# Optimization experiments

Hardware: AMD Instinct MI355X
Metric: run time of the kernel (lower is better)

Reference implementation:

```python
import jax, jax.numpy as jnp
import numpy as np

E = 4          # num_experts
M = 4          # num_modals
C = 512        # in_channels
H1, H2, OUT = 128, 48, 16  # expert hidden/output channels


def setup_inputs() -> dict:
    key = jax.random.key(0)
    ks = jax.random.split(key, 8)
    b, n, t = 16, 4096, 1

    def w(k, shape, fan_in):
        return jax.random.normal(k, shape, jnp.float32) * (1.0 / np.sqrt(fan_in))

    return {
        "x": jax.random.normal(ks[0], (b, C, M, n, t), jnp.float32),
        # stacked expert params: leading axis = expert
        "W1": w(ks[1], (E, H1, C), C),   "b1": jnp.zeros((E, H1), jnp.float32),
        "W2": w(ks[2], (E, H2, H1), H1), "b2": jnp.zeros((E, H2), jnp.float32),
        "W3": w(ks[3], (E, OUT, H2), H2),"b3": jnp.zeros((E, OUT), jnp.float32),
        # gate params
        "Wg1": w(ks[4], (H1, C), C),     "bg1": jnp.zeros((H1,), jnp.float32),
        "Wg2": w(ks[5], (E, H1), H1),    "bg2": jnp.zeros((E,), jnp.float32),
    }


def reference(x, W1, b1, W2, b2, W3, b3, Wg1, bg1, Wg2, bg2):
    b = x.shape[0]
    # gate: AdaptiveAvgPool3d((M,1,1)) == mean over (n,t) since m==M already
    pooled = x.mean(axis=(3, 4))                                   # (b, C, M)
    g = jax.nn.relu(jnp.einsum('oc,bcm->bom', Wg1, pooled) + bg1[None, :, None])
    g = jnp.einsum('oc,bcm->bom', Wg2, g) + bg2[None, :, None]     # (b, E, M)
    # torch: flatten then view(b, num_modals, num_experts) -> row-major reshape
    weights = jax.nn.softmax(g.reshape(b, M, E), axis=2)           # (b, M, E)

    # all experts densely: 1x1x1 convs == channel matmuls, stacked over e
    h = jax.nn.relu(jnp.einsum('eoc,bcmnt->ebomnt', W1, x)
                    + b1[:, None, :, None, None, None])            # (E,b,H1,M,n,t)
    h = jax.nn.relu(jnp.einsum('eoi,ebimnt->ebomnt', W2, h)
                    + b2[:, None, :, None, None, None])            # (E,b,H2,M,n,t)
    h = (jnp.einsum('eoi,ebimnt->ebomnt', W3, h)
         + b3[:, None, :, None, None, None])                       # (E,b,OUT,M,n,t)

    # per-modal weighted combination over experts
    out = jnp.einsum('ebomnt,bme->bomnt', h, weights)              # (b,OUT,M,n,t)
    return out
```

## Files before the change

kernel.cpp:

```cpp
#include <hip/hip_runtime.h>

typedef _Float16 f16;
typedef f16 f16x8 __attribute__((ext_vector_type(8)));
typedef f16 f16x4 __attribute__((ext_vector_type(4)));
typedef f16 f16x2 __attribute__((ext_vector_type(2)));
typedef float f32x4 __attribute__((ext_vector_type(4)));

#define BDIM 16
#define CDIM 512
#define MDIM 4
#define NDIM 4096
#define NB   64
#define NTILES (NDIM/NB)
#define NBMT  (BDIM*MDIM*NTILES)

#define SX(p) ((((p)&7) ^ (((p)>>3)&7)))

__global__ __launch_bounds__(256) void prep_kernel(
    const float* __restrict__ W1, const float* __restrict__ W2, const float* __restrict__ W3,
    f16* __restrict__ W1s, f16* __restrict__ W2s, f16* __restrict__ W3s)
{
  int i = blockIdx.x * 256 + threadIdx.x;
  if (i < 262144) {
    int ki = i & 7; int rest = i >> 3;
    int o = rest & 127; rest >>= 7;
    int kb = rest & 63; int e = rest >> 6;
    W1s[i] = (f16)W1[(e*128 + o)*512 + kb*8 + ki];
  } else if (i < 262144 + 24576) {
    int j = i - 262144;
    int ki = j & 7; int rest = j >> 3;
    int o = rest % 48; rest /= 48;
    int kb = rest & 15; int e = rest >> 4;
    W2s[j] = (f16)W2[(e*48 + o)*128 + kb*8 + ki];
  } else if (i < 262144 + 24576 + 4096) {
    int j = i - 262144 - 24576;
    int ki = j & 7; int rest = j >> 3;
    int o = rest & 15; rest >>= 4;
    int kb = rest & 7; int e = rest >> 3;
    int k = kb*8 + ki;
    W3s[j] = (k < 48) ? (f16)W3[(e*16 + o)*48 + k] : (f16)0.f;
  }
}

__global__ __launch_bounds__(1024, 4) void moe_kernel(
    const float* __restrict__ x,
    const f16* __restrict__ W1s, const f16* __restrict__ W2s, const f16* __restrict__ W3s,
    const float* __restrict__ b1, const float* __restrict__ b2, const float* __restrict__ b3,
    float* __restrict__ partial, f16* __restrict__ h3)
{
  extern __shared__ char smem[];
  char* H1t = smem;
  char* H2t = smem + 65536;

  const int tid  = threadIdx.x;
  const int bid  = blockIdx.x;
  const int tile = bid & 63;
  const int m    = (bid >> 6) & 3;
  const int b    = bid >> 8;

  const int wave = tid >> 6, lane = tid & 63;
  const int g = lane >> 4, r = lane & 15;
  const int eh = wave >> 3;
  const int o0 = (wave & 7) * 16;

  {
    uint4 z = make_uint4(0u,0u,0u,0u);
    ((uint4*)H2t)[tid] = z;
    ((uint4*)H2t)[tid + 1024] = z;
  }

  const int cp0 = tid >> 4;
  const int q   = tid & 15;
  const size_t xrow = ((size_t)(b*2048 + m))*4096 + (size_t)tile*64 + (size_t)(q*4);

  #pragma unroll
  for (int it = 0; it < 2; ++it) {
    const int cp = cp0 + it*64;
    const int c  = 2*cp;
    f32x4 v0 = *(const f32x4*)(x + xrow + (size_t)c*16384);
    f32x4 v1 = *(const f32x4*)(x + xrow + (size_t)(c+1)*16384);
    #pragma unroll
    for (int i = 0; i < 4; ++i) {
      int p = q*4 + i;
      f16x2 hv; hv[0] = (f16)v0[i]; hv[1] = (f16)v1[i];
      *(f16x2*)(smem + p*512 + ((4*cp) ^ (SX(p)<<4))) = hv;
    }
    float s0 = v0[0]+v0[1]+v0[2]+v0[3];
    float s1 = v1[0]+v1[1]+v1[2]+v1[3];
    #pragma unroll
    for (int off = 8; off; off >>= 1) {
      s0 += __shfl_down(s0, off, 16);
      s1 += __shfl_down(s1, off, 16);
    }
    if (q == 0) { float2 sv = {s0, s1}; *(float2*)(partial + (size_t)bid*512 + c) = sv; }
  }
  __syncthreads();

  f32x4 acc[2][4];
  #pragma unroll
  for (int i = 0; i < 2; ++i)
    #pragma unroll
    for (int pt = 0; pt < 4; ++pt) acc[i][pt] = (f32x4){0.f,0.f,0.f,0.f};

  auto compute_half = [&](const char* Xb, int h) {
    #pragma unroll
    for (int ks = 0; ks < 8; ++ks) {
      const int kbh = ks*4 + g;
      const int kbg = h*32 + kbh;
      f16x8 bf[4];
      #pragma unroll
      for (int pt = 0; pt < 4; ++pt) {
        int p = pt*16 + r;
        bf[pt] = *(const f16x8*)(Xb + p*512 + ((kbh*16) ^ (SX(p)<<4)));
      }
      #pragma unroll
      for (int i = 0; i < 2; ++i) {
        const int e = eh*2 + i;
        f16x8 a = *(const f16x8*)(W1s + ((size_t)((e*64 + kbg)*128) + o0 + r)*8);
        acc[i][0] = __builtin_amdgcn_mfma_f32_16x16x32_f16(a, bf[0], acc[i][0], 0, 0, 0);
        acc[i][1] = __builtin_amdgcn_mfma_f32_16x16x32_f16(a, bf[1], acc[i][1], 0, 0, 0);
        acc[i][2] = __builtin_amdgcn_mfma_f32_16x16x32_f16(a, bf[2], acc[i][2], 0, 0, 0);
        acc[i][3] = __builtin_amdgcn_mfma_f32_16x16x32_f16(a, bf[3], acc[i][3], 0, 0, 0);
      }
    }
  };

  f32x4 nva0, nva1, nvb0, nvb1;
  {
    const int ca = 256 + 2*cp0;
    const int cb = 256 + 2*(cp0 + 64);
    nva0 = *(const f32x4*)(x + xrow + (size_t)ca*16384);
    nva1 = *(const f32x4*)(x + xrow + (size_t)(ca+1)*16384);
    nvb0 = *(const f32x4*)(x + xrow + (size_t)cb*16384);
    nvb1 = *(const f32x4*)(x + xrow + (size_t)(cb+1)*16384);
  }
  compute_half(smem, 0);

  {
    char* X1 = smem + 32768;
    #pragma unroll
    for (int i = 0; i < 4; ++i) {
      int p = q*4 + i;
      f16x2 ha; ha[0] = (f16)nva0[i]; ha[1] = (f16)nva1[i];
      *(f16x2*)(X1 + p*512 + ((4*cp0) ^ (SX(p)<<4))) = ha;
      f16x2 hb; hb[0] = (f16)nvb0[i]; hb[1] = (f16)nvb1[i];
      *(f16x2*)(X1 + p*512 + ((4*(cp0+64)) ^ (SX(p)<<4))) = hb;
    }
    float sa0 = nva0[0]+nva0[1]+nva0[2]+nva0[3];
    float sa1 = nva1[0]+nva1[1]+nva1[2]+nva1[3];
    float sb0 = nvb0[0]+nvb0[1]+nvb0[2]+nvb0[3];
    float sb1 = nvb1[0]+nvb1[1]+nvb1[2]+nvb1[3];
    #pragma unroll
    for (int off = 8; off; off >>= 1) {
      sa0 += __shfl_down(sa0, off, 16);
      sa1 += __shfl_down(sa1, off, 16);
      sb0 += __shfl_down(sb0, off, 16);
      sb1 += __shfl_down(sb1, off, 16);
    }
    if (q == 0) {
      float2 sva = {sa0, sa1};
      float2 svb = {sb0, sb1};
      *(float2*)(partial + (size_t)bid*512 + 256 + 2*cp0)       = sva;
      *(float2*)(partial + (size_t)bid*512 + 256 + 2*(cp0+64))  = svb;
    }
  }
  __syncthreads();
  compute_half(smem + 32768, 1);
  __syncthreads();

  #pragma unroll
  for (int i = 0; i < 2; ++i) {
    const int e = eh*2 + i;
    const f32x4 bias = *(const f32x4*)(b1 + e*128 + o0 + g*4);
    const int colb = (o0 + g*4)*2;
    #pragma unroll
    for (int pt = 0; pt < 4; ++pt) {
      int p = pt*16 + r;
      f16x4 hv;
      #pragma unroll
      for (int j = 0; j < 4; ++j) hv[j] = (f16)fmaxf(acc[i][pt][j] + bias[j], 0.f);
      *(f16x4*)(H1t + e*16384 + p*256 + (colb ^ (SX(p)<<4))) = hv;
    }
  }
  __syncthreads();

  #pragma unroll
  for (int s = 0; s < 3; ++s) {
    const int f  = wave*3 + s;
    const int e  = f / 12;
    const int ot = (f % 12) >> 2;
    const int pt = f & 3;
    const int p  = pt*16 + r;
    f32x4 acc2 = {0.f,0.f,0.f,0.f};
    #pragma unroll
    for (int ks = 0; ks < 4; ++ks) {
      const int kb = ks*4 + g;
      f16x8 a  = *(const f16x8*)(W2s + (size_t)((e*16 + kb)*48 + ot*16 + r)*8);
      f16x8 bf = *(const f16x8*)(H1t + e*16384 + p*256 + ((kb*16) ^ (SX(p)<<4)));
      acc2 = __builtin_amdgcn_mfma_f32_16x16x32_f16(a, bf, acc2, 0, 0, 0);
    }
    const f32x4 bias = *(const f32x4*)(b2 + e*48 + ot*16 + g*4);
    const int colb = (ot*16 + g*4)*2;
    f16x4 hv;
    #pragma unroll
    for (int j = 0; j < 4; ++j) hv[j] = (f16)fmaxf(acc2[j] + bias[j], 0.f);
    *(f16x4*)(H2t + e*8192 + p*128 + (colb ^ (SX(p)<<4))) = hv;
  }
  __syncthreads();

  {
    const int e  = wave >> 2;
    const int pt = wave & 3;
    const int p  = pt*16 + r;
    f32x4 acc3 = {0.f,0.f,0.f,0.f};
    #pragma unroll
    for (int ks = 0; ks < 2; ++ks) {
      const int kb = ks*4 + g;
      f16x8 a  = *(const f16x8*)(W3s + (size_t)((e*8 + kb)*16 + r)*8);
      f16x8 bf = *(const f16x8*)(H2t + e*8192 + p*128 + ((kb*16) ^ (SX(p)<<4)));
      acc3 = __builtin_amdgcn_mfma_f32_16x16x32_f16(a, bf, acc3, 0, 0, 0);
    }
    const f32x4 bias = *(const f32x4*)(b3 + e*16 + g*4);
    #pragma unroll
    for (int j = 0; j < 4; ++j) {
      int o = g*4 + j;
      h3[(((size_t)(e*NBMT + bid))*16 + o)*64 + pt*16 + r] = (f16)(acc3[j] + bias[j]);
    }
  }
}

__global__ __launch_bounds__(256) void gate_kernel(
    const float* __restrict__ partial, const float* __restrict__ Wg1,
    const float* __restrict__ bg1, const float* __restrict__ Wg2,
    const float* __restrict__ bg2, float* __restrict__ wgt)
{
  __shared__ float pl[512*4];
  __shared__ float g1[128*4];
  __shared__ float g2[16];
  const int b = blockIdx.x, tid = threadIdx.x;

  const int c0 = tid * 2;
  #pragma unroll
  for (int mm = 0; mm < 4; ++mm) {
    const float* base = partial + ((size_t)((b*4 + mm)*64))*512 + c0;
    float a0 = 0.f, a1 = 0.f;
    for (int tl = 0; tl < 64; ++tl) {
      float2 v = *(const float2*)(base + tl*512);
      a0 += v.x; a1 += v.y;
    }
    pl[(c0+0)*4 + mm] = a0 * (1.0f/4096.0f);
    pl[(c0+1)*4 + mm] = a1 * (1.0f/4096.0f);
  }
  __syncthreads();

  #pragma unroll
  for (int u = 0; u < 2; ++u) {
    int idx = u*256 + tid;
    int o = idx >> 2, mm = idx & 3;
    float acc = bg1[o];
    for (int c = 0; c < 512; ++c) acc += Wg1[o*512 + c] * pl[c*4 + mm];
    g1[o*4 + mm] = fmaxf(acc, 0.f);
  }
  __syncthreads();
  if (tid < 16) {
    int e = tid >> 2, mm = tid & 3;
    float acc = bg2[e];
    for (int o = 0; o < 128; ++o) acc += Wg2[e*128 + o] * g1[o*4 + mm];
    g2[e*4 + mm] = acc;
  }
  __syncthreads();
  if (tid < 4) {
    int mrow = tid;
    float v0 = g2[mrow*4+0], v1 = g2[mrow*4+1], v2 = g2[mrow*4+2], v3 = g2[mrow*4+3];
    float mx = fmaxf(fmaxf(v0,v1), fmaxf(v2,v3));
    float e0 = expf(v0-mx), e1 = expf(v1-mx), e2 = expf(v2-mx), e3 = expf(v3-mx);
    float inv = 1.0f / (e0+e1+e2+e3);
    wgt[b*16 + mrow*4 + 0] = e0*inv;
    wgt[b*16 + mrow*4 + 1] = e1*inv;
    wgt[b*16 + mrow*4 + 2] = e2*inv;
    wgt[b*16 + mrow*4 + 3] = e3*inv;
  }
}

__global__ __launch_bounds__(256) void combine_kernel(
    const f16* __restrict__ h3, const float* __restrict__ wgt,
    float* __restrict__ out)
{
  const int bmt = blockIdx.x;
  const int tile = bmt & 63, m = (bmt >> 6) & 3, b = bmt >> 8;
  const int t = threadIdx.x;
  const int o = t >> 4, pq = t & 15;

  const f32x4 w = *(const f32x4*)(wgt + (b*4 + m)*4);
  f32x4 s = {0.f, 0.f, 0.f, 0.f};
  #pragma unroll
  for (int e = 0; e < 4; ++e) {
    f16x4 h = *(const f16x4*)(h3 + (((size_t)(e*NBMT + bmt))*16 + o)*64 + pq*4);
    #pragma unroll
    for (int j = 0; j < 4; ++j) s[j] += w[e] * (float)h[j];
  }
  *(f32x4*)(out + (((size_t)b*16 + o)*4 + m)*4096 + tile*64 + pq*4) = s;
}

extern "C" void kernel_launch(void* const* d_in, const int* in_sizes, int n_in,
                              void* d_out, int out_size, void* d_ws, size_t ws_size,
                              hipStream_t stream) {
  const float* x   = (const float*)d_in[0];
  const float* W1  = (const float*)d_in[1];
  const float* b1  = (const float*)d_in[2];
  const float* W2  = (const float*)d_in[3];
  const float* b2  = (const float*)d_in[4];
  const float* W3  = (const float*)d_in[5];
  const float* b3  = (const float*)d_in[6];
  const float* Wg1 = (const float*)d_in[7];
  const float* bg1 = (const float*)d_in[8];
  const float* Wg2 = (const float*)d_in[9];
  const float* bg2 = (const float*)d_in[10];
  float* out = (float*)d_out;

  char* ws = (char*)d_ws;
  float* wgt    = (float*)ws;
  f16* W1s      = (f16*)(ws + 4096);
  f16* W2s      = (f16*)(ws + 4096 + 524288);
  f16* W3s      = (f16*)(ws + 4096 + 524288 + 49152);
  float* partial= (float*)(ws + (1u<<20));
  f16* h3       = (f16*)(ws + (16u<<20));

  hipFuncSetAttribute(reinterpret_cast<const void*>(moe_kernel),
                      hipFuncAttributeMaxDynamicSharedMemorySize, 98304);

  prep_kernel<<<(262144 + 24576 + 4096 + 255)/256, 256, 0, stream>>>(W1, W2, W3, W1s, W2s, W3s);
  moe_kernel<<<NBMT, 1024, 98304, stream>>>(x, W1s, W2s, W3s, b1, b2, b3, partial, h3);
  gate_kernel<<<BDIM, 256, 0, stream>>>(partial, Wg1, bg1, Wg2, bg2, wgt);
  combine_kernel<<<NBMT, 256, 0, stream>>>(h3, wgt, out);
}
```

Before: 419.4 us.

## Pre-transpose x to f16, compute gate first, fuse combine into persistent MoE kernel

A new xprep kernel converts x to an f16 tile-major layout and computes the channel sums for pooling. The gate then runs before the MoE kernel, so the MoE kernel can apply the softmax weights directly and write the final output, removing the h3 intermediate and the combine kernel. The MoE kernel is now persistent: 256 blocks each loop over 16 tiles, double-buffering the next f16 tile from global memory through registers into shared memory. The cost is an extra f16 round trip of x through global memory and fewer blocks, each using more shared memory.

New measurement: 813.7 us. 1.94x slower.

```diff
diff --git a/kernel.cpp b/kernel.cpp
--- a/kernel.cpp
+++ b/kernel.cpp
@@ -3,18 +3,16 @@
 typedef _Float16 f16;
 typedef f16 f16x8 __attribute__((ext_vector_type(8)));
 typedef f16 f16x4 __attribute__((ext_vector_type(4)));
-typedef f16 f16x2 __attribute__((ext_vector_type(2)));
 typedef float f32x4 __attribute__((ext_vector_type(4)));
 
 #define BDIM 16
-#define CDIM 512
 #define MDIM 4
 #define NDIM 4096
 #define NB   64
 #define NTILES (NDIM/NB)
 #define NBMT  (BDIM*MDIM*NTILES)
 
-#define SX(p) ((((p)&7) ^ (((p)>>3)&7)))
+#define MFMA16(a,b,c) __builtin_amdgcn_mfma_f32_16x16x32_f16(a, b, c, 0, 0, 0)
 
 __global__ __launch_bounds__(256) void prep_kernel(
     const float* __restrict__ W1, const float* __restrict__ W2, const float* __restrict__ W3,
@@ -42,191 +40,50 @@
   }
 }
 
-__global__ __launch_bounds__(1024, 4) void moe_kernel(
-    const float* __restrict__ x,
-    const f16* __restrict__ W1s, const f16* __restrict__ W2s, const f16* __restrict__ W3s,
-    const float* __restrict__ b1, const float* __restrict__ b2, const float* __restrict__ b3,
-    float* __restrict__ partial, f16* __restrict__ h3)
+__global__ __launch_bounds__(256) void xprep_kernel(
+    const float* __restrict__ x, f16* __restrict__ Xt, float* __restrict__ partial)
 {
-  extern __shared__ char smem[];
-  char* H1t = smem;
-  char* H2t = smem + 65536;
-
-  const int tid  = threadIdx.x;
-  const int bid  = blockIdx.x;
-  const int tile = bid & 63;
-  const int m    = (bid >> 6) & 3;
-  const int b    = bid >> 8;
-
-  const int wave = tid >> 6, lane = tid & 63;
-  const int g = lane >> 4, r = lane & 15;
-  const int eh = wave >> 3;
-  const int o0 = (wave & 7) * 16;
-
-  {
-    uint4 z = make_uint4(0u,0u,0u,0u);
-    ((uint4*)H2t)[tid] = z;
-    ((uint4*)H2t)[tid + 1024] = z;
-  }
-
-  const int cp0 = tid >> 4;
-  const int q   = tid & 15;
-  const size_t xrow = ((size_t)(b*2048 + m))*4096 + (size_t)tile*64 + (size_t)(q*4);
+  const int bid = blockIdx.x;
+  const int cb  = bid & 63;
+  const int bm  = bid >> 6;
+  const int b   = bm >> 2, m = bm & 3;
+  const int t   = threadIdx.x;
+  const int lane = t & 63, wid = t >> 6;
+
+  __shared__ float red[4][8];
+  float s[8] = {0.f,0.f,0.f,0.f,0.f,0.f,0.f,0.f};
 
   #pragma unroll
-  for (int it = 0; it < 2; ++it) {
-    const int cp = cp0 + it*64;
-    const int c  = 2*cp;
-    f32x4 v0 = *(const f32x4*)(x + xrow + (size_t)c*16384);
-    f32x4 v1 = *(const f32x4*)(x + xrow + (size_t)(c+1)*16384);
+  for (int pass = 0; pass < 4; ++pass) {
+    const int n0 = pass*1024 + t*4;
+    f32x4 v[8];
+    #pragma unroll
+    for (int ci = 0; ci < 8; ++ci)
+      v[ci] = *(const f32x4*)(x + (((size_t)(b*512 + cb*8 + ci))*4 + m)*4096 + n0);
+    #pragma unroll
+    for (int ci = 0; ci < 8; ++ci)
+      s[ci] += v[ci][0] + v[ci][1] + v[ci][2] + v[ci][3];
+    const int tile = n0 >> 6, p = n0 & 63;
+    const size_t obase = (((size_t)bm*64 + tile)*64 + cb)*64;
     #pragma unroll
     for (int i = 0; i < 4; ++i) {
-      int p = q*4 + i;
-      f16x2 hv; hv[0] = (f16)v0[i]; hv[1] = (f16)v1[i];
-      *(f16x2*)(smem + p*512 + ((4*cp) ^ (SX(p)<<4))) = hv;
-    }
-    float s0 = v0[0]+v0[1]+v0[2]+v0[3];
-    float s1 = v1[0]+v1[1]+v1[2]+v1[3];
-    #pragma unroll
-    for (int off = 8; off; off >>= 1) {
-      s0 += __shfl_down(s0, off, 16);
-      s1 += __shfl_down(s1, off, 16);
-    }
-    if (q == 0) { float2 sv = {s0, s1}; *(float2*)(partial + (size_t)bid*512 + c) = sv; }
-  }
+      f16x8 o;
+      #pragma unroll
+      for (int ci = 0; ci < 8; ++ci) o[ci] = (f16)v[ci][i];
+      *(f16x8*)(Xt + (obase + p + i)*8) = o;
+    }
+  }
+
+  #pragma unroll
+  for (int off = 32; off; off >>= 1)
+    #pragma unroll
+    for (int ci = 0; ci < 8; ++ci) s[ci] += __shfl_down(s[ci], off);
+  if (lane == 0)
+    #pragma unroll
+    for (int ci = 0; ci < 8; ++ci) red[wid][ci] = s[ci];
   __syncthreads();
-
-  f32x4 acc[2][4];
-  #pragma unroll
-  for (int i = 0; i < 2; ++i)
-    #pragma unroll
-    for (int pt = 0; pt < 4; ++pt) acc[i][pt] = (f32x4){0.f,0.f,0.f,0.f};
-
-  auto compute_half = [&](const char* Xb, int h) {
-    #pragma unroll
-    for (int ks = 0; ks < 8; ++ks) {
-      const int kbh = ks*4 + g;
-      const int kbg = h*32 + kbh;
-      f16x8 bf[4];
-      #pragma unroll
-      for (int pt = 0; pt < 4; ++pt) {
-        int p = pt*16 + r;
-        bf[pt] = *(const f16x8*)(Xb + p*512 + ((kbh*16) ^ (SX(p)<<4)));
-      }
-      #pragma unroll
-      for (int i = 0; i < 2; ++i) {
-        const int e = eh*2 + i;
-        f16x8 a = *(const f16x8*)(W1s + ((size_t)((e*64 + kbg)*128) + o0 + r)*8);
-        acc[i][0] = __builtin_amdgcn_mfma_f32_16x16x32_f16(a, bf[0], acc[i][0], 0, 0, 0);
-        acc[i][1] = __builtin_amdgcn_mfma_f32_16x16x32_f16(a, bf[1], acc[i][1], 0, 0, 0);
-        acc[i][2] = __builtin_amdgcn_mfma_f32_16x16x32_f16(a, bf[2], acc[i][2], 0, 0, 0);
-        acc[i][3] = __builtin_amdgcn_mfma_f32_16x16x32_f16(a, bf[3], acc[i][3], 0, 0, 0);
-      }
-    }
-  };
-
-  f32x4 nva0, nva1, nvb0, nvb1;
-  {
-    const int ca = 256 + 2*cp0;
-    const int cb = 256 + 2*(cp0 + 64);
-    nva0 = *(const f32x4*)(x + xrow + (size_t)ca*16384);
-    nva1 = *(const f32x4*)(x + xrow + (size_t)(ca+1)*16384);
-    nvb0 = *(const f32x4*)(x + xrow + (size_t)cb*16384);
-    nvb1 = *(const f32x4*)(x + xrow + (size_t)(cb+1)*16384);
-  }
-  compute_half(smem, 0);
-
-  {
-    char* X1 = smem + 32768;
-    #pragma unroll
-    for (int i = 0; i < 4; ++i) {
-      int p = q*4 + i;
-      f16x2 ha; ha[0] = (f16)nva0[i]; ha[1] = (f16)nva1[i];
-      *(f16x2*)(X1 + p*512 + ((4*cp0) ^ (SX(p)<<4))) = ha;
-      f16x2 hb; hb[0] = (f16)nvb0[i]; hb[1] = (f16)nvb1[i];
-      *(f16x2*)(X1 + p*512 + ((4*(cp0+64)) ^ (SX(p)<<4))) = hb;
-    }
-    float sa0 = nva0[0]+nva0[1]+nva0[2]+nva0[3];
-    float sa1 = nva1[0]+nva1[1]+nva1[2]+nva1[3];
-    float sb0 = nvb0[0]+nvb0[1]+nvb0[2]+nvb0[3];
-    float sb1 = nvb1[0]+nvb1[1]+nvb1[2]+nvb1[3];
-    #pragma unroll
-    for (int off = 8; off; off >>= 1) {
-      sa0 += __shfl_down(sa0, off, 16);
-      sa1 += __shfl_down(sa1, off, 16);
-      sb0 += __shfl_down(sb0, off, 16);
-      sb1 += __shfl_down(sb1, off, 16);
-    }
-    if (q == 0) {
-      float2 sva = {sa0, sa1};
-      float2 svb = {sb0, sb1};
-      *(float2*)(partial + (size_t)bid*512 + 256 + 2*cp0)       = sva;
-      *(float2*)(partial + (size_t)bid*512 + 256 + 2*(cp0+64))  = svb;
-    }
-  }
-  __syncthreads();
-  compute_half(smem + 32768, 1);
-  __syncthreads();
-
-  #pragma unroll
-  for (int i = 0; i < 2; ++i) {
-    const int e = eh*2 + i;
-    const f32x4 bias = *(const f32x4*)(b1 + e*128 + o0 + g*4);
-    const int colb = (o0 + g*4)*2;
-    #pragma unroll
-    for (int pt = 0; pt < 4; ++pt) {
-      int p = pt*16 + r;
-      f16x4 hv;
-      #pragma unroll
-      for (int j = 0; j < 4; ++j) hv[j] = (f16)fmaxf(acc[i][pt][j] + bias[j], 0.f);
-      *(f16x4*)(H1t + e*16384 + p*256 + (colb ^ (SX(p)<<4))) = hv;
-    }
-  }
-  __syncthreads();
-
-  #pragma unroll
-  for (int s = 0; s < 3; ++s) {
-    const int f  = wave*3 + s;
-    const int e  = f / 12;
-    const int ot = (f % 12) >> 2;
-    const int pt = f & 3;
-    const int p  = pt*16 + r;
-    f32x4 acc2 = {0.f,0.f,0.f,0.f};
-    #pragma unroll
-    for (int ks = 0; ks < 4; ++ks) {
-      const int kb = ks*4 + g;
-      f16x8 a  = *(const f16x8*)(W2s + (size_t)((e*16 + kb)*48 + ot*16 + r)*8);
-      f16x8 bf = *(const f16x8*)(H1t + e*16384 + p*256 + ((kb*16) ^ (SX(p)<<4)));
-      acc2 = __builtin_amdgcn_mfma_f32_16x16x32_f16(a, bf, acc2, 0, 0, 0);
-    }
-    const f32x4 bias = *(const f32x4*)(b2 + e*48 + ot*16 + g*4);
-    const int colb = (ot*16 + g*4)*2;
-    f16x4 hv;
-    #pragma unroll
-    for (int j = 0; j < 4; ++j) hv[j] = (f16)fmaxf(acc2[j] + bias[j], 0.f);
-    *(f16x4*)(H2t + e*8192 + p*128 + (colb ^ (SX(p)<<4))) = hv;
-  }
-  __syncthreads();
-
-  {
-    const int e  = wave >> 2;
-    const int pt = wave & 3;
-    const int p  = pt*16 + r;
-    f32x4 acc3 = {0.f,0.f,0.f,0.f};
-    #pragma unroll
-    for (int ks = 0; ks < 2; ++ks) {
-      const int kb = ks*4 + g;
-      f16x8 a  = *(const f16x8*)(W3s + (size_t)((e*8 + kb)*16 + r)*8);
-      f16x8 bf = *(const f16x8*)(H2t + e*8192 + p*128 + ((kb*16) ^ (SX(p)<<4)));
-      acc3 = __builtin_amdgcn_mfma_f32_16x16x32_f16(a, bf, acc3, 0, 0, 0);
-    }
-    const f32x4 bias = *(const f32x4*)(b3 + e*16 + g*4);
-    #pragma unroll
-    for (int j = 0; j < 4; ++j) {
-      int o = g*4 + j;
-      h3[(((size_t)(e*NBMT + bid))*16 + o)*64 + pt*16 + r] = (f16)(acc3[j] + bias[j]);
-    }
-  }
+  if (t < 8)
+    partial[(size_t)bm*512 + cb*8 + t] = red[0][t] + red[1][t] + red[2][t] + red[3][t];
 }
 
 __global__ __launch_bounds__(256) void gate_kernel(
@@ -238,21 +95,11 @@
   __shared__ float g1[128*4];
   __shared__ float g2[16];
   const int b = blockIdx.x, tid = threadIdx.x;
-
-  const int c0 = tid * 2;
-  #pragma unroll
-  for (int mm = 0; mm < 4; ++mm) {
-    const float* base = partial + ((size_t)((b*4 + mm)*64))*512 + c0;
-    float a0 = 0.f, a1 = 0.f;
-    for (int tl = 0; tl < 64; ++tl) {
-      float2 v = *(const float2*)(base + tl*512);
-      a0 += v.x; a1 += v.y;
-    }
-    pl[(c0+0)*4 + mm] = a0 * (1.0f/4096.0f);
-    pl[(c0+1)*4 + mm] = a1 * (1.0f/4096.0f);
+  for (int i = tid; i < 2048; i += 256) {
+    int c = i >> 2, mm = i & 3;
+    pl[c*4 + mm] = partial[(size_t)(b*4 + mm)*512 + c] * (1.0f/4096.0f);
   }
   __syncthreads();
-
   #pragma unroll
   for (int u = 0; u < 2; ++u) {
     int idx = u*256 + tid;
@@ -282,24 +129,145 @@
   }
 }
 
-__global__ __launch_bounds__(256) void combine_kernel(
-    const f16* __restrict__ h3, const float* __restrict__ wgt,
-    float* __restrict__ out)
+__global__ __launch_bounds__(1024, 4) void moe_kernel(
+    const f16* __restrict__ Xt,
+    const f16* __restrict__ W1s, const f16* __restrict__ W2s, const f16* __restrict__ W3s,
+    const float* __restrict__ b1, const float* __restrict__ b2, const float* __restrict__ b3,
+    const float* __restrict__ wgt, float* __restrict__ out)
 {
-  const int bmt = blockIdx.x;
-  const int tile = bmt & 63, m = (bmt >> 6) & 3, b = bmt >> 8;
-  const int t = threadIdx.x;
-  const int o = t >> 4, pq = t & 15;
-
-  const f32x4 w = *(const f32x4*)(wgt + (b*4 + m)*4);
-  f32x4 s = {0.f, 0.f, 0.f, 0.f};
-  #pragma unroll
-  for (int e = 0; e < 4; ++e) {
-    f16x4 h = *(const f16x4*)(h3 + (((size_t)(e*NBMT + bmt))*16 + o)*64 + pq*4);
-    #pragma unroll
-    for (int j = 0; j < 4; ++j) s[j] += w[e] * (float)h[j];
-  }
-  *(f32x4*)(out + (((size_t)b*16 + o)*4 + m)*4096 + tile*64 + pq*4) = s;
+  extern __shared__ __align__(16) char smem[];
+  char* H2 = smem + 131072;
+
+  const int tid  = threadIdx.x;
+  const int wave = tid >> 6, lane = tid & 63;
+  const int g = lane >> 4, r = lane & 15;
+  const int eh = wave >> 3;
+  const int o0 = (wave & 7) * 16;
+
+  if (tid < 512) {
+    int e = tid >> 7, off = tid & 127;
+    *(uint4*)(H2 + e*8192 + 6144 + off*16) = make_uint4(0u,0u,0u,0u);
+  }
+
+  const int bmt0 = blockIdx.x * 16;
+  {
+    const uint4* src = (const uint4*)(Xt + (size_t)bmt0 * 32768);
+    #pragma unroll
+    for (int j = 0; j < 4; ++j)
+      *(uint4*)(smem + tid*16 + j*16384) = src[tid + j*1024];
+  }
+  int cur = 0;
+
+  #pragma unroll 1
+  for (int it = 0; it < 16; ++it) {
+    const int bmt  = bmt0 + it;
+    const int tile = bmt & 63, m = (bmt >> 6) & 3, b = bmt >> 8;
+    char* Xcur = smem + cur*65536;
+    char* Xoth = smem + (cur^1)*65536;
+
+    uint4 pf0, pf1, pf2, pf3;
+    if (it < 15) {
+      const uint4* src = (const uint4*)(Xt + (size_t)(bmt+1) * 32768);
+      pf0 = src[tid]; pf1 = src[tid+1024]; pf2 = src[tid+2048]; pf3 = src[tid+3072];
+    }
+    __syncthreads();
+
+    f32x4 acc[2][4];
+    #pragma unroll
+    for (int i = 0; i < 2; ++i)
+      #pragma unroll
+      for (int pt = 0; pt < 4; ++pt) acc[i][pt] = (f32x4){0.f,0.f,0.f,0.f};
+
+    #pragma unroll
+    for (int ks = 0; ks < 16; ++ks) {
+      const int kb = ks*4 + g;
+      f16x8 bf[4];
+      #pragma unroll
+      for (int pt = 0; pt < 4; ++pt)
+        bf[pt] = *(const f16x8*)(Xcur + (kb*64 + pt*16 + r)*16);
+      #pragma unroll
+      for (int i = 0; i < 2; ++i) {
+        const int e = eh*2 + i;
+        f16x8 a = *(const f16x8*)(W1s + ((size_t)((e*64 + kb)*128) + o0 + r)*8);
+        acc[i][0] = MFMA16(a, bf[0], acc[i][0]);
+        acc[i][1] = MFMA16(a, bf[1], acc[i][1]);
+        acc[i][2] = MFMA16(a, bf[2], acc[i][2]);
+        acc[i][3] = MFMA16(a, bf[3], acc[i][3]);
+      }
+    }
+    __syncthreads();
+
+    #pragma unroll
+    for (int i = 0; i < 2; ++i) {
+      const int e = eh*2 + i;
+      const f32x4 bias = *(const f32x4*)(b1 + e*128 + o0 + g*4);
+      const int ob = (o0 >> 3) + (g >> 1);
+      #pragma unroll
+      for (int pt = 0; pt < 4; ++pt) {
+        const int p = pt*16 + r;
+        f16x4 hv;
+        #pragma unroll
+        for (int j = 0; j < 4; ++j) hv[j] = (f16)fmaxf(acc[i][pt][j] + bias[j], 0.f);
+        *(f16x4*)(Xcur + e*16384 + (ob*64 + p)*16 + (g&1)*8) = hv;
+      }
+    }
+    __syncthreads();
+
+    #pragma unroll
+    for (int s = 0; s < 3; ++s) {
+      const int f  = wave*3 + s;
+      const int e  = f / 12, ot = (f % 12) >> 2, pt = f & 3;
+      const int p  = pt*16 + r;
+      f32x4 a2 = {0.f,0.f,0.f,0.f};
+      #pragma unroll
+      for (int ks = 0; ks < 4; ++ks) {
+        const int kb = ks*4 + g;
+        f16x8 a  = *(const f16x8*)(W2s + (size_t)((e*16 + kb)*48 + ot*16 + r)*8);
+        f16x8 bf = *(const f16x8*)(Xcur + e*16384 + (kb*64 + p)*16);
+        a2 = MFMA16(a, bf, a2);
+      }
+      const f32x4 bias = *(const f32x4*)(b2 + e*48 + ot*16 + g*4);
+      const int hb = ot*2 + (g >> 1);
+      f16x4 hv;
+      #pragma unroll
+      for (int j = 0; j < 4; ++j) hv[j] = (f16)fmaxf(a2[j] + bias[j], 0.f);
+      *(f16x4*)(H2 + e*8192 + (hb*64 + p)*16 + (g&1)*8) = hv;
+    }
+    __syncthreads();
+
+    if (wave < 4) {
+      const int pt = wave, p = pt*16 + r;
+      f32x4 sacc = {0.f,0.f,0.f,0.f};
+      #pragma unroll
+      for (int e = 0; e < 4; ++e) {
+        f32x4 a3 = {0.f,0.f,0.f,0.f};
+        #pragma unroll
+        for (int ks = 0; ks < 2; ++ks) {
+          const int kb = ks*4 + g;
+          f16x8 a  = *(const f16x8*)(W3s + (size_t)((e*8 + kb)*16 + r)*8);
+          f16x8 bf = *(const f16x8*)(H2 + e*8192 + (kb*64 + p)*16);
+          a3 = MFMA16(a, bf, a3);
+        }
+        const float we = wgt[(b*4 + m)*4 + e];
+        const f32x4 bv = *(const f32x4*)(b3 + e*16 + g*4);
+        #pragma unroll
+        for (int j = 0; j < 4; ++j) sacc[j] += we * (a3[j] + bv[j]);
+      }
+      #pragma unroll
+      for (int j = 0; j < 4; ++j) {
+        const int o = g*4 + j;
+        out[(((size_t)b*16 + o)*4 + m)*4096 + (size_t)tile*64 + p] = sacc[j];
+      }
+    }
+
+    if (it < 15) {
+      *(uint4*)(Xoth + tid*16)         = pf0;
+      *(uint4*)(Xoth + tid*16 + 16384) = pf1;
+      *(uint4*)(Xoth + tid*16 + 32768) = pf2;
+      *(uint4*)(Xoth + tid*16 + 49152) = pf3;
+    }
+    cur ^= 1;
+  }
 }
 
 extern "C" void kernel_launch(void* const* d_in, const int* in_sizes, int n_in,
@@ -319,18 +287,18 @@
   float* out = (float*)d_out;
 
   char* ws = (char*)d_ws;
-  float* wgt    = (float*)ws;
-  f16* W1s      = (f16*)(ws + 4096);
-  f16* W2s      = (f16*)(ws + 4096 + 524288);
-  f16* W3s      = (f16*)(ws + 4096 + 524288 + 49152);
-  float* partial= (float*)(ws + (1u<<20));
-  f16* h3       = (f16*)(ws + (16u<<20));
+  float* wgt     = (float*)ws;
+  f16*   W1s     = (f16*)(ws + 4096);
+  f16*   W2s     = (f16*)(ws + 4096 + 524288);
+  f16*   W3s     = (f16*)(ws + 4096 + 524288 + 49152);
+  float* partial = (float*)(ws + (1u<<20));
+  f16*   Xt      = (f16*)(ws + (16u<<20));
 
   hipFuncSetAttribute(reinterpret_cast<const void*>(moe_kernel),
-                      hipFuncAttributeMaxDynamicSharedMemorySize, 98304);
+                      hipFuncAttributeMaxDynamicSharedMemorySize, 163840);
 
   prep_kernel<<<(262144 + 24576 + 4096 + 255)/256, 256, 0, stream>>>(W1, W2, W3, W1s, W2s, W3s);
-  moe_kernel<<<NBMT, 1024, 98304, stream>>>(x, W1s, W2s, W3s, b1, b2, b3, partial, h3);
+  xprep_kernel<<<64*64, 256, 0, stream>>>(x, Xt, partial);
   gate_kernel<<<BDIM, 256, 0, stream>>>(partial, Wg1, bg1, Wg2, bg2, wgt);
-  combine_kernel<<<NBMT, 256, 0, stream>>>(h3, wgt, out);
-}
+  moe_kernel<<<256, 1024, 163840, stream>>>(Xt, W1s, W2s, W3s, b1, b2, b3, wgt, out);
+}
```
